# Kernel optimization log

Measured on AMD Instinct MI355X. Metric: run time of the kernel, lower is better.

The kernel has to match this reference:

```python
import jax, jax.numpy as jnp
import numpy as np

C = 256      # channels (multiple of 32 for GroupNorm)
K = 3        # kernel
PAD = 1      # padding
G = 32       # GroupNorm groups
EPS = 1e-5


def setup_inputs() -> dict:
    key = jax.random.key(0)
    ks = jax.random.split(key, 7)
    B, H, W = 4, 64, 64
    return {
        "x": jax.random.normal(ks[0], (B, C, H, W), jnp.float32),
        "offset": jax.random.normal(ks[1], (B, 2 * K * K, H, W), jnp.float32),
        "weight": jax.random.normal(ks[2], (C, C, K, K), jnp.float32) * 0.01,
        "att_w": jax.random.normal(ks[3], (1, C), jnp.float32) * 0.01,
        "att_b": jnp.zeros((1,), jnp.float32),
        "gamma": jnp.ones((C,), jnp.float32),
        "beta": jnp.zeros((C,), jnp.float32),
    }


def _bilinear_one(xb, py, px):
    # xb: [C, H, W]; py, px: [KK, H, W] fractional sample coords (zero-pad outside)
    H, W = xb.shape[1], xb.shape[2]
    y0 = jnp.floor(py)
    x0 = jnp.floor(px)
    y1 = y0 + 1.0
    x1 = x0 + 1.0
    wy1 = py - y0
    wy0 = 1.0 - wy1
    wx1 = px - x0
    wx0 = 1.0 - wx1

    def g(yi, xi):
        valid = (yi >= 0) & (yi < H) & (xi >= 0) & (xi < W)
        yc = jnp.clip(yi, 0, H - 1).astype(jnp.int32)
        xc = jnp.clip(xi, 0, W - 1).astype(jnp.int32)
        return xb[:, yc, xc] * valid[None].astype(xb.dtype)  # [C, KK, H, W]

    return (g(y0, x0) * (wy0 * wx0)[None] + g(y0, x1) * (wy0 * wx1)[None]
            + g(y1, x0) * (wy1 * wx0)[None] + g(y1, x1) * (wy1 * wx1)[None])


def reference(x, offset, weight, att_w, att_b, gamma, beta):
    B, Cc, H, W = x.shape
    KK = K * K
    off = offset.reshape(B, KK, 2, H, W)  # (dy, dx) per kernel tap
    ii, jj = jnp.meshgrid(jnp.arange(K), jnp.arange(K), indexing='ij')
    dky = (ii - PAD).reshape(KK).astype(x.dtype)
    dkx = (jj - PAD).reshape(KK).astype(x.dtype)
    ys = jnp.arange(H, dtype=x.dtype)
    xs = jnp.arange(W, dtype=x.dtype)
    # sample coords [B, KK, H, W]
    py = ys[None, :, None] + dky[:, None, None] + off[:, :, 0]
    px = xs[None, None, :] + dkx[:, None, None] + off[:, :, 1]

    # deformable unfold: [B, C, KK, H, W]
    xu = jax.vmap(_bilinear_one)(x, py, px)

    # max over kernel taps -> channel attention gate
    xm = xu.max(axis=2)  # [B, C, H, W]
    att = jax.nn.sigmoid(jnp.einsum('bchw,oc->bohw', xm, att_w)
                         + att_b[None, :, None, None])  # [B, 1, H, W]

    # gate the unfolded samples, then emulate the conv as one GEMM
    xw = xu * att[:, :, None]  # broadcast over C, KK
    cols = xw.transpose(1, 2, 0, 3, 4).reshape(Cc * KK, B * H * W)  # [C*KK, BHW]
    out = (weight.reshape(Cc, Cc * KK) @ cols).reshape(Cc, B, H, W).transpose(1, 0, 2, 3)

    # GroupNorm(32, C) + ReLU
    og = out.reshape(B, G, Cc // G, H, W)
    mu = og.mean(axis=(2, 3, 4), keepdims=True)
    var = og.var(axis=(2, 3, 4), keepdims=True)
    on = ((og - mu) * jax.lax.rsqrt(var + EPS)).reshape(B, Cc, H, W)
    return jax.nn.relu(on * gamma[None, :, None, None] + beta[None, :, None, None])
```

## Files before the change

kernel.cpp:

```cpp
#include <hip/hip_runtime.h>

#define CT 256
#define KDIM 2304
#define COLP 296

typedef unsigned short u16;
typedef __attribute__((ext_vector_type(8))) short bf16x8;
typedef __attribute__((ext_vector_type(4))) float f32x4;
typedef __fp16 fp16x2 __attribute__((ext_vector_type(2)));

__device__ __forceinline__ unsigned f2b(float f) {
    unsigned u = __float_as_uint(f);
    u += 0x7fffu + ((u >> 16) & 1u);
    return u >> 16;
}
__device__ __forceinline__ float lo_bf(unsigned u) { return __uint_as_float(u << 16); }
__device__ __forceinline__ float hi_bf(unsigned u) { return __uint_as_float(u & 0xffff0000u); }

__device__ __forceinline__ void gload_lds16(const uint4* g, u16* l) {
    __builtin_amdgcn_global_load_lds((const __attribute__((address_space(1))) void*)g,
                                     (__attribute__((address_space(3))) void*)l, 16, 0, 0);
}

__global__ __launch_bounds__(256) void k_prep(const float* __restrict__ x, uint4* __restrict__ xi,
                                              const float* __restrict__ wgt, uint4* __restrict__ pw)
{
    if (blockIdx.x < 2048) {
        int u = blockIdx.x * 256 + threadIdx.x;
        int bcg = u >> 12, p = u & 4095;
        const float* xp = x + (((size_t)bcg) << 15) + p;
        unsigned r[4];
#pragma unroll
        for (int i = 0; i < 4; ++i) {
            float a = xp[(size_t)(2 * i) << 12];
            float c = xp[(size_t)(2 * i + 1) << 12];
            r[i] = f2b(a) | (f2b(c) << 16);
        }
        uint4 o; o.x = r[0]; o.y = r[1]; o.z = r[2]; o.w = r[3];
        xi[u] = o;
    } else {
        int u = (blockIdx.x - 2048) * 256 + threadIdx.x;
        int kc = u >> 10, rm = u & 1023;
        int m = rm >> 2, j = rm & 3;
        int round = kc / 9, tap = kc - round * 9;
        const float* src = wgt + (size_t)m * KDIM + tap;
        int c0 = round * 32 + j * 8;
        unsigned q[4];
#pragma unroll
        for (int i = 0; i < 4; ++i) {
            float a = src[(size_t)(c0 + 2 * i) * 9];
            float c = src[(size_t)(c0 + 2 * i + 1) * 9];
            q[i] = f2b(a) | (f2b(c) << 16);
        }
        uint4 o; o.x = q[0]; o.y = q[1]; o.z = q[2]; o.w = q[3];
        pw[u] = o;
    }
}

__global__ __launch_bounds__(512, 2) void k_main(const uint4* __restrict__ xi, const float* __restrict__ off,
                                                 const uint4* __restrict__ pw, const float* __restrict__ att_w,
                                                 const float* __restrict__ att_b,
                                                 float* __restrict__ outp, float* __restrict__ gnpart)
{
    __shared__ uint2 s_wt[288];
    __shared__ int2 s_off[288];
    __shared__ u16 Xs[4 * 6656];
    __shared__ u16 col[32 * COLP];
    __shared__ float s_att[32];

    int rowblk = blockIdx.x >> 1, half = blockIdx.x & 1;
    int b = rowblk >> 6, h = rowblk & 63, n0 = half * 32;
    int tid = threadIdx.x;
    int lane = tid & 63, w = tid >> 6;
    int l15 = lane & 15, kb = lane >> 4;
    int wm = w * 32;

    for (int e = tid; e < 288; e += 512) {
        int kk = e >> 5, wl = e & 31;
        int ww_ = n0 + wl;
        int ky = kk / 3, kx = kk - ky * 3;
        float dy = off[((size_t)(b * 18 + 2 * kk) * 64 + h) * 64 + ww_];
        float dx = off[((size_t)(b * 18 + 2 * kk + 1) * 64 + h) * 64 + ww_];
        float py = (float)(h + ky - 1) + dy;
        float px = (float)(ww_ + kx - 1) + dx;
        float y0f = floorf(py), x0f = floorf(px);
        int y0 = (int)y0f, x0 = (int)x0f;
        float fy = py - y0f, fx = px - x0f;
        float vy0 = (y0 >= 0 && y0 < 64) ? 1.f : 0.f;
        float vy1 = (y0 >= -1 && y0 < 63) ? 1.f : 0.f;
        float vx0 = (x0 >= 0 && x0 < 64) ? 1.f : 0.f;
        float vx1 = (x0 >= -1 && x0 < 63) ? 1.f : 0.f;
        float w0 = (1.f - fy) * (1.f - fx) * vy0 * vx0;
        float w1 = (1.f - fy) * fx * vy0 * vx1;
        float w2 = fy * (1.f - fx) * vy1 * vx0;
        float w3 = fy * fx * vy1 * vx1;
        fp16x2 pA = __builtin_amdgcn_cvt_pkrtz(w0, w1);
        fp16x2 pB = __builtin_amdgcn_cvt_pkrtz(w2, w3);
        uint2 wp;
        wp.x = __builtin_bit_cast(unsigned, pA);
        wp.y = __builtin_bit_cast(unsigned, pB);
        int yc0 = min(max(y0, 0), 63), yc1 = min(max(y0 + 1, 0), 63);
        int xc0 = min(max(x0, 0), 63), xc1 = min(max(x0 + 1, 0), 63);
        s_wt[e] = wp;
        s_off[e] = make_int2((yc0 * 64 + xc0) | ((yc0 * 64 + xc1) << 16),
                             (yc1 * 64 + xc0) | ((yc1 * 64 + xc1) << 16));
    }

    int r0 = max(0, h - 6), r1 = min(63, h + 6);
    int nrows = r1 - r0 + 1, nw = nrows * 64, rbase = r0 * 64;
    size_t xib = (size_t)(b * 32) << 12;

    float att_acc = 0.f;
    f32x4 acc[2][2];
#pragma unroll
    for (int mt = 0; mt < 2; ++mt)
#pragma unroll
        for (int nt = 0; nt < 2; ++nt) acc[mt][nt] = (f32x4){0.f, 0.f, 0.f, 0.f};

#pragma unroll
    for (int cgl = 0; cgl < 2; ++cgl)
        for (int e = tid; e < nw; e += 512)
            gload_lds16(&xi[xib + ((size_t)cgl << 12) + rbase + e], &Xs[(cgl * 6656 + e * 8)]);

    for (int stage = 0; stage < 16; ++stage) {
        int buf = stage & 1;
        int s2 = stage & 1;
        __syncthreads();
        if (stage < 15) {
            size_t nb = xib + ((size_t)((stage + 1) * 2) << 12) + rbase;
#pragma unroll
            for (int cgl = 0; cgl < 2; ++cgl)
                for (int e = tid; e < nw; e += 512)
                    gload_lds16(&xi[nb + ((size_t)cgl << 12) + e],
                                &Xs[(((buf ^ 1) * 2 + cgl) * 6656 + e * 8)]);
        }
        for (int it = tid; it < 576; it += 512) {
            int cgl = (it >= 288) ? 1 : 0;
            int it2 = it - cgl * 288;
            int tap = it2 >> 5, nn = it2 & 31;
            int xsb = (buf * 2 + cgl) * 6656;
            size_t gfall = xib + ((size_t)(stage * 2 + cgl) << 12);
            uint2 wp = s_wt[it2];
            fp16x2 wA = __builtin_bit_cast(fp16x2, wp.x);
            fp16x2 wB = __builtin_bit_cast(fp16x2, wp.y);
            float wx = (float)wA[0], wy = (float)wA[1];
            float wz = (float)wB[0], ww2 = (float)wB[1];
            int2 of = s_off[it2];
            int P00 = of.x & 0xffff, P01 = (of.x >> 16) & 0xffff;
            int P10 = of.y & 0xffff, P11 = (of.y >> 16) & 0xffff;
            uint4 c00, c01, c10, c11;
            int Q;
            Q = P00 - rbase;
            if ((unsigned)Q < (unsigned)nw) c00 = *(const uint4*)&Xs[xsb + Q * 8]; else c00 = xi[gfall + P00];
            Q = P01 - rbase;
            if ((unsigned)Q < (unsigned)nw) c01 = *(const uint4*)&Xs[xsb + Q * 8]; else c01 = xi[gfall + P01];
            Q = P10 - rbase;
            if ((unsigned)Q < (unsigned)nw) c10 = *(const uint4*)&Xs[xsb + Q * 8]; else c10 = xi[gfall + P10];
            Q = P11 - rbase;
            if ((unsigned)Q < (unsigned)nw) c11 = *(const uint4*)&Xs[xsb + Q * 8]; else c11 = xi[gfall + P11];
            const unsigned* a00 = (const unsigned*)&c00;
            const unsigned* a01 = (const unsigned*)&c01;
            const unsigned* a10 = (const unsigned*)&c10;
            const unsigned* a11 = (const unsigned*)&c11;
            unsigned o[4];
#pragma unroll
            for (int q = 0; q < 4; ++q) {
                float v0 = wx * lo_bf(a00[q]) + wy * lo_bf(a01[q]) + wz * lo_bf(a10[q]) + ww2 * lo_bf(a11[q]);
                float v1 = wx * hi_bf(a00[q]) + wy * hi_bf(a01[q]) + wz * hi_bf(a10[q]) + ww2 * hi_bf(a11[q]);
                o[q] = f2b(v0) | (f2b(v1) << 16);
            }
            uint4 ov; ov.x = o[0]; ov.y = o[1]; ov.z = o[2]; ov.w = o[3];
            int sp = s2 * 2 + cgl;
            *(uint4*)&col[nn * COLP + tap * 32 + sp * 8] = ov;
        }

        if (stage & 1) {
            int round = stage >> 1;
            __syncthreads();

            if (tid < 64) {
                int nn = tid >> 1, h2 = tid & 1;
#pragma unroll
                for (int sp = 0; sp < 4; ++sp) {
                    const u16* base = &col[nn * COLP + sp * 8 + h2 * 4];
                    float m0 = -1e30f, m1 = -1e30f, m2 = -1e30f, m3 = -1e30f;
#pragma unroll
                    for (int t = 0; t < 9; ++t) {
                        uint2 v = *(const uint2*)(base + t * 32);
                        m0 = fmaxf(m0, lo_bf(v.x)); m1 = fmaxf(m1, hi_bf(v.x));
                        m2 = fmaxf(m2, lo_bf(v.y)); m3 = fmaxf(m3, hi_bf(v.y));
                    }
                    int cb = round * 32 + sp * 8 + h2 * 4;
                    att_acc += att_w[cb] * m0 + att_w[cb + 1] * m1 + att_w[cb + 2] * m2 + att_w[cb + 3] * m3;
                }
            }
#pragma unroll
            for (int ts = 0; ts < 9; ++ts) {
                int kc = round * 9 + ts;
                bf16x8 bf[2];
#pragma unroll
                for (int nt = 0; nt < 2; ++nt)
                    bf[nt] = *(const bf16x8*)&col[(nt * 16 + l15) * COLP + ts * 32 + kb * 8];
#pragma unroll
                for (int mt = 0; mt < 2; ++mt) {
                    uint4 a = pw[(size_t)kc * 1024 + (wm + mt * 16 + l15) * 4 + kb];
                    bf16x8 af = __builtin_bit_cast(bf16x8, a);
#pragma unroll
                    for (int nt = 0; nt < 2; ++nt)
                        acc[mt][nt] = __builtin_amdgcn_mfma_f32_16x16x32_bf16(af, bf[nt], acc[mt][nt], 0, 0, 0);
                }
            }
        }
    }

    if (tid < 64) {
        float v = att_acc + __shfl_xor(att_acc, 1);
        if ((tid & 1) == 0) s_att[tid >> 1] = 1.f / (1.f + expf(-(v + att_b[0])));
    }
    __syncthreads();

    float attn[2];
#pragma unroll
    for (int nt = 0; nt < 2; ++nt) attn[nt] = s_att[nt * 16 + l15];

#pragma unroll
    for (int mt = 0; mt < 2; ++mt) {
        float s1 = 0.f, s2 = 0.f;
#pragma unroll
        for (int nt = 0; nt < 2; ++nt)
#pragma unroll
            for (int r = 0; r < 4; ++r) {
                float v = acc[mt][nt][r] * attn[nt];
                int m = wm + mt * 16 + kb * 4 + r;
                outp[(((size_t)(b * CT + m)) << 12) + h * 64 + n0 + nt * 16 + l15] = v;
                s1 += v; s2 += v * v;
            }
#pragma unroll
        for (int d = 1; d <= 16; d <<= 1) {
            s1 += __shfl_xor(s1, d);
            s2 += __shfl_xor(s2, d);
        }
        if ((lane & 31) == 0) {
            int gidx = w * 4 + mt * 2 + (kb >> 1);
            gnpart[blockIdx.x * 64 + gidx * 2] = s1;
            gnpart[blockIdx.x * 64 + gidx * 2 + 1] = s2;
        }
    }
}

__global__ __launch_bounds__(256) void k_gn(const float* __restrict__ gnpart, const float* __restrict__ gamma,
                                            const float* __restrict__ beta, float* __restrict__ outp)
{
    __shared__ float rs1[128], rs2[128];
    __shared__ float s_stat[2];
    int bg = blockIdx.x;
    int b = bg >> 5, g = bg & 31;
    int tid = threadIdx.x;
    if (tid < 128) {
        int blk = (b * 64 + (tid >> 1)) * 2 + (tid & 1);
        rs1[tid] = gnpart[blk * 64 + g * 2];
        rs2[tid] = gnpart[blk * 64 + g * 2 + 1];
    }
    __syncthreads();
    if (tid < 64) {
        float a = rs1[tid] + rs1[tid + 64];
        float c = rs2[tid] + rs2[tid + 64];
#pragma unroll
        for (int d = 1; d <= 32; d <<= 1) {
            a += __shfl_xor(a, d);
            c += __shfl_xor(c, d);
        }
        if (tid == 0) {
            float mean = a * (1.f / 32768.f);
            float var = c * (1.f / 32768.f) - mean * mean;
            s_stat[0] = mean;
            s_stat[1] = rsqrtf(var + 1e-5f);
        }
    }
    __syncthreads();
    float mean = s_stat[0], rstd = s_stat[1];
    float4* p4 = (float4*)(outp + ((size_t)(b * CT + g * 8) << 12));
    for (int i = tid; i < 8192; i += 256) {
        int c = g * 8 + (i >> 10);
        float ga = gamma[c], be = beta[c];
        float4 v = p4[i];
        float4 r;
        r.x = fmaxf((v.x - mean) * rstd * ga + be, 0.f);
        r.y = fmaxf((v.y - mean) * rstd * ga + be, 0.f);
        r.z = fmaxf((v.z - mean) * rstd * ga + be, 0.f);
        r.w = fmaxf((v.w - mean) * rstd * ga + be, 0.f);
        p4[i] = r;
    }
}

extern "C" void kernel_launch(void* const* d_in, const int* in_sizes, int n_in,
                              void* d_out, int out_size, void* d_ws, size_t ws_size,
                              hipStream_t stream)
{
    const float* x = (const float*)d_in[0];
    const float* off = (const float*)d_in[1];
    const float* wgt = (const float*)d_in[2];
    const float* attw = (const float*)d_in[3];
    const float* attb = (const float*)d_in[4];
    const float* gamma = (const float*)d_in[5];
    const float* beta = (const float*)d_in[6];
    float* outp = (float*)d_out;

    char* ws = (char*)d_ws;
    uint4* xi = (uint4*)ws;
    uint4* pw = (uint4*)(ws + 8388608);
    float* gnpart = (float*)(ws + 9568256);

    k_prep<<<dim3(2336), dim3(256), 0, stream>>>(x, xi, wgt, pw);
    k_main<<<dim3(512), dim3(512), 0, stream>>>(xi, off, pw, attw, attb, outp, gnpart);
    k_gn<<<dim3(128), dim3(256), 0, stream>>>(gnpart, gamma, beta, outp);
}
```

Measured before the change: 150.1 us.

## Switch intermediate storage and MFMA from bf16 to fp16 with packed-half bilinear math

```diff
diff --git a/kernel.cpp b/kernel.cpp
--- a/kernel.cpp
+++ b/kernel.cpp
@@ -5,17 +5,14 @@
 #define COLP 296
 
 typedef unsigned short u16;
-typedef __attribute__((ext_vector_type(8))) short bf16x8;
+typedef _Float16 h2 __attribute__((ext_vector_type(2)));
+typedef _Float16 h8 __attribute__((ext_vector_type(8)));
 typedef __attribute__((ext_vector_type(4))) float f32x4;
-typedef __fp16 fp16x2 __attribute__((ext_vector_type(2)));
-
-__device__ __forceinline__ unsigned f2b(float f) {
-    unsigned u = __float_as_uint(f);
-    u += 0x7fffu + ((u >> 16) & 1u);
-    return u >> 16;
-}
-__device__ __forceinline__ float lo_bf(unsigned u) { return __uint_as_float(u << 16); }
-__device__ __forceinline__ float hi_bf(unsigned u) { return __uint_as_float(u & 0xffff0000u); }
+
+__device__ __forceinline__ unsigned pkh(float a, float b) {
+    h2 r; r[0] = (_Float16)a; r[1] = (_Float16)b;
+    return __builtin_bit_cast(unsigned, r);
+}
 
 __device__ __forceinline__ void gload_lds16(const uint4* g, u16* l) {
     __builtin_amdgcn_global_load_lds((const __attribute__((address_space(1))) void*)g,
@@ -31,11 +28,8 @@
         const float* xp = x + (((size_t)bcg) << 15) + p;
         unsigned r[4];
 #pragma unroll
-        for (int i = 0; i < 4; ++i) {
-            float a = xp[(size_t)(2 * i) << 12];
-            float c = xp[(size_t)(2 * i + 1) << 12];
-            r[i] = f2b(a) | (f2b(c) << 16);
-        }
+        for (int i = 0; i < 4; ++i)
+            r[i] = pkh(xp[(size_t)(2 * i) << 12], xp[(size_t)(2 * i + 1) << 12]);
         uint4 o; o.x = r[0]; o.y = r[1]; o.z = r[2]; o.w = r[3];
         xi[u] = o;
     } else {
@@ -47,14 +41,50 @@
         int c0 = round * 32 + j * 8;
         unsigned q[4];
 #pragma unroll
-        for (int i = 0; i < 4; ++i) {
-            float a = src[(size_t)(c0 + 2 * i) * 9];
-            float c = src[(size_t)(c0 + 2 * i + 1) * 9];
-            q[i] = f2b(a) | (f2b(c) << 16);
-        }
+        for (int i = 0; i < 4; ++i)
+            q[i] = pkh(src[(size_t)(c0 + 2 * i) * 9], src[(size_t)(c0 + 2 * i + 1) * 9]);
         uint4 o; o.x = q[0]; o.y = q[1]; o.z = q[2]; o.w = q[3];
         pw[u] = o;
     }
+}
+
+__device__ __forceinline__ void gather_one(int it2, int sp, int xsb, size_t gfall,
+                                           const uint2* s_wt, const int2* s_off,
+                                           const u16* Xs, u16* col,
+                                           const uint4* __restrict__ xi, int rbase, int nw)
+{
+    int tap = it2 >> 5, nn = it2 & 31;
+    uint2 wp = s_wt[it2];
+    h2 w01 = __builtin_bit_cast(h2, wp.x);
+    h2 w23 = __builtin_bit_cast(h2, wp.y);
+    h2 wxp = (h2){w01[0], w01[0]}, wyp = (h2){w01[1], w01[1]};
+    h2 wzp = (h2){w23[0], w23[0]}, wwp = (h2){w23[1], w23[1]};
+    int2 of = s_off[it2];
+    int P00 = of.x & 0xffff, P01 = (of.x >> 16) & 0xffff;
+    int P10 = of.y & 0xffff, P11 = (of.y >> 16) & 0xffff;
+    uint4 c00, c01, c10, c11;
+    int Q;
+    Q = P00 - rbase;
+    if ((unsigned)Q < (unsigned)nw) c00 = *(const uint4*)&Xs[xsb + Q * 8]; else c00 = xi[gfall + P00];
+    Q = P01 - rbase;
+    if ((unsigned)Q < (unsigned)nw) c01 = *(const uint4*)&Xs[xsb + Q * 8]; else c01 = xi[gfall + P01];
+    Q = P10 - rbase;
+    if ((unsigned)Q < (unsigned)nw) c10 = *(const uint4*)&Xs[xsb + Q * 8]; else c10 = xi[gfall + P10];
+    Q = P11 - rbase;
+    if ((unsigned)Q < (unsigned)nw) c11 = *(const uint4*)&Xs[xsb + Q * 8]; else c11 = xi[gfall + P11];
+    const unsigned* a00 = (const unsigned*)&c00;
+    const unsigned* a01 = (const unsigned*)&c01;
+    const unsigned* a10 = (const unsigned*)&c10;
+    const unsigned* a11 = (const unsigned*)&c11;
+    unsigned o[4];
+#pragma unroll
+    for (int q = 0; q < 4; ++q) {
+        h2 r = wxp * __builtin_bit_cast(h2, a00[q]) + wyp * __builtin_bit_cast(h2, a01[q])
+             + wzp * __builtin_bit_cast(h2, a10[q]) + wwp * __builtin_bit_cast(h2, a11[q]);
+        o[q] = __builtin_bit_cast(unsigned, r);
+    }
+    uint4 ov; ov.x = o[0]; ov.y = o[1]; ov.z = o[2]; ov.w = o[3];
+    *(uint4*)&col[nn * COLP + tap * 32 + sp * 8] = ov;
 }
 
 __global__ __launch_bounds__(512, 2) void k_main(const uint4* __restrict__ xi, const float* __restrict__ off,
@@ -94,11 +124,9 @@
         float w1 = (1.f - fy) * fx * vy0 * vx1;
         float w2 = fy * (1.f - fx) * vy1 * vx0;
         float w3 = fy * fx * vy1 * vx1;
-        fp16x2 pA = __builtin_amdgcn_cvt_pkrtz(w0, w1);
-        fp16x2 pB = __builtin_amdgcn_cvt_pkrtz(w2, w3);
         uint2 wp;
-        wp.x = __builtin_bit_cast(unsigned, pA);
-        wp.y = __builtin_bit_cast(unsigned, pB);
+        wp.x = pkh(w0, w1);
+        wp.y = pkh(w2, w3);
         int yc0 = min(max(y0, 0), 63), yc1 = min(max(y0 + 1, 0), 63);
         int xc0 = min(max(x0, 0), 63), xc1 = min(max(x0 + 1, 0), 63);
         s_wt[e] = wp;
@@ -134,44 +162,16 @@
                     gload_lds16(&xi[nb + ((size_t)cgl << 12) + e],
                                 &Xs[(((buf ^ 1) * 2 + cgl) * 6656 + e * 8)]);
         }
-        for (int it = tid; it < 576; it += 512) {
+        {
+            int it = tid;
             int cgl = (it >= 288) ? 1 : 0;
-            int it2 = it - cgl * 288;
-            int tap = it2 >> 5, nn = it2 & 31;
-            int xsb = (buf * 2 + cgl) * 6656;
-            size_t gfall = xib + ((size_t)(stage * 2 + cgl) << 12);
-            uint2 wp = s_wt[it2];
-            fp16x2 wA = __builtin_bit_cast(fp16x2, wp.x);
-            fp16x2 wB = __builtin_bit_cast(fp16x2, wp.y);
-            float wx = (float)wA[0], wy = (float)wA[1];
-            float wz = (float)wB[0], ww2 = (float)wB[1];
-            int2 of = s_off[it2];
-            int P00 = of.x & 0xffff, P01 = (of.x >> 16) & 0xffff;
-            int P10 = of.y & 0xffff, P11 = (of.y >> 16) & 0xffff;
-            uint4 c00, c01, c10, c11;
-            int Q;
-            Q = P00 - rbase;
-            if ((unsigned)Q < (unsigned)nw) c00 = *(const uint4*)&Xs[xsb + Q * 8]; else c00 = xi[gfall + P00];
-            Q = P01 - rbase;
-            if ((unsigned)Q < (unsigned)nw) c01 = *(const uint4*)&Xs[xsb + Q * 8]; else c01 = xi[gfall + P01];
-            Q = P10 - rbase;
-            if ((unsigned)Q < (unsigned)nw) c10 = *(const uint4*)&Xs[xsb + Q * 8]; else c10 = xi[gfall + P10];
-            Q = P11 - rbase;
-            if ((unsigned)Q < (unsigned)nw) c11 = *(const uint4*)&Xs[xsb + Q * 8]; else c11 = xi[gfall + P11];
-            const unsigned* a00 = (const unsigned*)&c00;
-            const unsigned* a01 = (const unsigned*)&c01;
-            const unsigned* a10 = (const unsigned*)&c10;
-            const unsigned* a11 = (const unsigned*)&c11;
-            unsigned o[4];
-#pragma unroll
-            for (int q = 0; q < 4; ++q) {
-                float v0 = wx * lo_bf(a00[q]) + wy * lo_bf(a01[q]) + wz * lo_bf(a10[q]) + ww2 * lo_bf(a11[q]);
-                float v1 = wx * hi_bf(a00[q]) + wy * hi_bf(a01[q]) + wz * hi_bf(a10[q]) + ww2 * hi_bf(a11[q]);
-                o[q] = f2b(v0) | (f2b(v1) << 16);
+            gather_one(it - cgl * 288, s2 * 2 + cgl, (buf * 2 + cgl) * 6656,
+                       xib + ((size_t)(stage * 2 + cgl) << 12), s_wt, s_off, Xs, col, xi, rbase, nw);
+            if (tid >= 448) {
+                int it2 = tid + 64;
+                gather_one(it2 - 288, s2 * 2 + 1, (buf * 2 + 1) * 6656,
+                           xib + ((size_t)(stage * 2 + 1) << 12), s_wt, s_off, Xs, col, xi, rbase, nw);
             }
-            uint4 ov; ov.x = o[0]; ov.y = o[1]; ov.z = o[2]; ov.w = o[3];
-            int sp = s2 * 2 + cgl;
-            *(uint4*)&col[nn * COLP + tap * 32 + sp * 8] = ov;
         }
 
         if (stage & 1) {
@@ -179,35 +179,37 @@
             __syncthreads();
 
             if (tid < 64) {
-                int nn = tid >> 1, h2 = tid & 1;
+                int nn = tid >> 1, h2i = tid & 1;
 #pragma unroll
                 for (int sp = 0; sp < 4; ++sp) {
-                    const u16* base = &col[nn * COLP + sp * 8 + h2 * 4];
+                    const u16* base = &col[nn * COLP + sp * 8 + h2i * 4];
                     float m0 = -1e30f, m1 = -1e30f, m2 = -1e30f, m3 = -1e30f;
 #pragma unroll
                     for (int t = 0; t < 9; ++t) {
                         uint2 v = *(const uint2*)(base + t * 32);
-                        m0 = fmaxf(m0, lo_bf(v.x)); m1 = fmaxf(m1, hi_bf(v.x));
-                        m2 = fmaxf(m2, lo_bf(v.y)); m3 = fmaxf(m3, hi_bf(v.y));
+                        h2 va = __builtin_bit_cast(h2, v.x);
+                        h2 vb = __builtin_bit_cast(h2, v.y);
+                        m0 = fmaxf(m0, (float)va[0]); m1 = fmaxf(m1, (float)va[1]);
+                        m2 = fmaxf(m2, (float)vb[0]); m3 = fmaxf(m3, (float)vb[1]);
                     }
-                    int cb = round * 32 + sp * 8 + h2 * 4;
+                    int cb = round * 32 + sp * 8 + h2i * 4;
                     att_acc += att_w[cb] * m0 + att_w[cb + 1] * m1 + att_w[cb + 2] * m2 + att_w[cb + 3] * m3;
                 }
             }
 #pragma unroll
             for (int ts = 0; ts < 9; ++ts) {
                 int kc = round * 9 + ts;
-                bf16x8 bf[2];
+                h8 bf[2];
 #pragma unroll
                 for (int nt = 0; nt < 2; ++nt)
-                    bf[nt] = *(const bf16x8*)&col[(nt * 16 + l15) * COLP + ts * 32 + kb * 8];
+                    bf[nt] = *(const h8*)&col[(nt * 16 + l15) * COLP + ts * 32 + kb * 8];
 #pragma unroll
                 for (int mt = 0; mt < 2; ++mt) {
                     uint4 a = pw[(size_t)kc * 1024 + (wm + mt * 16 + l15) * 4 + kb];
-                    bf16x8 af = __builtin_bit_cast(bf16x8, a);
+                    h8 af = __builtin_bit_cast(h8, a);
 #pragma unroll
                     for (int nt = 0; nt < 2; ++nt)
-                        acc[mt][nt] = __builtin_amdgcn_mfma_f32_16x16x32_bf16(af, bf[nt], acc[mt][nt], 0, 0, 0);
+                        acc[mt][nt] = __builtin_amdgcn_mfma_f32_16x16x32_f16(af, bf[nt], acc[mt][nt], 0, 0, 0);
                 }
             }
         }
```

Result: no change. 149.1 us (-0.7%).
